# Kernel optimization log

Hardware: AMD Instinct MI355X
Metric: run time of the kernel (lower is better)

Reference implementation:

```python
import jax, jax.numpy as jnp
import numpy as np

B, N, C = 4, 2048, 81
IMG_W, IMG_H = 1024.0, 800.0
SCORE_THRESH = 0.05
NMS_THRESH = 0.5
DETS_PER_IMG = 100
BBOX_XFORM_CLIP = float(np.log(1000.0 / 16.0))
WX, WY, WW, WH = 10.0, 10.0, 5.0, 5.0


def _make_boxes(key, n):
    k1, k2, k3, k4 = jax.random.split(key, 4)
    x1 = jax.random.uniform(k1, (n,)) * (IMG_W - 60.0)
    y1 = jax.random.uniform(k2, (n,)) * (IMG_H - 60.0)
    w = 10.0 + jax.random.uniform(k3, (n,)) * 300.0
    h = 10.0 + jax.random.uniform(k4, (n,)) * 300.0
    return jnp.stack([x1, y1, jnp.minimum(x1 + w, IMG_W - 1.0), jnp.minimum(y1 + h, IMG_H - 1.0)], axis=-1)


def setup_inputs() -> dict:
    key = jax.random.key(0)
    k1, k2, k3, k4 = jax.random.split(key, 4)
    return {
        "class_logits": jax.random.normal(k1, (B * N, C), jnp.float32),
        "box_regression": jax.random.normal(k2, (B * N, C * 8), jnp.float32) * 0.5,
        "left_proposals": _make_boxes(k3, B * N),
        "right_proposals": _make_boxes(k4, B * N),
    }


def decode(rel, boxes):
    widths = boxes[:, 2] - boxes[:, 0] + 1.0
    heights = boxes[:, 3] - boxes[:, 1] + 1.0
    ctr_x = boxes[:, 0] + 0.5 * widths
    ctr_y = boxes[:, 1] + 0.5 * heights
    dx = rel[:, 0::4] / WX
    dy = rel[:, 1::4] / WY
    dw = jnp.minimum(rel[:, 2::4] / WW, BBOX_XFORM_CLIP)
    dh = jnp.minimum(rel[:, 3::4] / WH, BBOX_XFORM_CLIP)
    pcx = dx * widths[:, None] + ctr_x[:, None]
    pcy = dy * heights[:, None] + ctr_y[:, None]
    pw = jnp.exp(dw) * widths[:, None]
    ph = jnp.exp(dh) * heights[:, None]
    x1 = pcx - 0.5 * pw
    y1 = pcy - 0.5 * ph
    x2 = pcx + 0.5 * pw - 1.0
    y2 = pcy + 0.5 * ph - 1.0
    return jnp.stack([x1, y1, x2, y2], axis=-1)  # [M, C, 4]


def clip_boxes(b):
    x1 = jnp.clip(b[..., 0], 0.0, IMG_W - 1.0)
    y1 = jnp.clip(b[..., 1], 0.0, IMG_H - 1.0)
    x2 = jnp.clip(b[..., 2], 0.0, IMG_W - 1.0)
    y2 = jnp.clip(b[..., 3], 0.0, IMG_H - 1.0)
    return jnp.stack([x1, y1, x2, y2], axis=-1)


def pairwise_iou(b):
    area = jnp.clip(b[:, 2] - b[:, 0] + 1.0, 0.0) * jnp.clip(b[:, 3] - b[:, 1] + 1.0, 0.0)
    lt = jnp.maximum(b[:, None, :2], b[None, :, :2])
    rb = jnp.minimum(b[:, None, 2:], b[None, :, 2:])
    wh = jnp.clip(rb - lt + 1.0, 0.0)
    inter = wh[..., 0] * wh[..., 1]
    return inter / jnp.maximum(area[:, None] + area[None, :] - inter, 1e-6)


def nms_keep(boxes, scores):
    # greedy NMS -> boolean keep mask (fixed shape)
    n = scores.shape[0]
    order = jnp.argsort(-scores)
    iou = pairwise_iou(boxes[order])
    idx = jnp.arange(n)
    def body(i, keep):
        sup = (iou[i] > NMS_THRESH) & keep[i] & (idx > i)
        return keep & (~sup)
    keep = jax.lax.fori_loop(0, n, body, jnp.ones((n,), bool))
    return jnp.zeros((n,), bool).at[order].set(keep)


def _per_image(prob, lb, rb):
    # prob [N,C], lb/rb [N,C,4]
    labels = jnp.argmax(prob, axis=-1)
    ar = jnp.arange(prob.shape[0])
    score = prob[ar, labels]
    lbox = lb[ar, labels]
    rbox = rb[ar, labels]
    valid = (labels >= 1) & (score > SCORE_THRESH)
    s = jnp.where(valid, score, -jnp.inf)
    keep = nms_keep(lbox, s) & nms_keep(rbox, s) & valid
    ms = jnp.where(keep, score, -jnp.inf)
    kth = jax.lax.top_k(ms, DETS_PER_IMG)[0][-1]
    keep = keep & (ms >= kth)
    return lbox, rbox, score, keep


def reference(class_logits, box_regression, left_proposals, right_proposals):
    prob = jax.nn.softmax(class_logits, axis=-1)  # [B*N, C]
    reg = box_regression.reshape(-1, C, 8)
    lb = clip_boxes(decode(reg[:, :, :4].reshape(-1, C * 4), left_proposals))
    rb = clip_boxes(decode(reg[:, :, 4:].reshape(-1, C * 4), right_proposals))
    prob = prob.reshape(B, N, C)
    lb = lb.reshape(B, N, C, 4)
    rb = rb.reshape(B, N, C, 4)
    lbox, rbox, score, keep = jax.vmap(_per_image)(prob, lb, rb)
    m = keep[..., None].astype(score.dtype)
    out = jnp.concatenate([lbox * m, rbox * m, jnp.where(keep, score, 0.0)[..., None]], axis=-1)
    return out  # [B, N, 9]
```

## Files before the change

kernel.cpp:

```cpp
#include <hip/hip_runtime.h>
#include <math.h>

#define NPROP 2048
#define NIMG 4
#define NCLS 81
#define REGW 648
#define SCORE_THRESH 0.05f
#define NMS_T 0.5f
#define DETS 100
#define XC 1023.0f
#define YC 799.0f
#define BBOX_CLIP 4.135166556742356f
#define NBIN 8192
#define SEL 320
#define MAXC 512
#define WRD 8
#define TRIP 2560

typedef unsigned long long u64;

__device__ __forceinline__ float areaf(float4 v) {
  return fmaxf(v.z - v.x + 1.0f, 0.0f) * fmaxf(v.w - v.y + 1.0f, 0.0f);
}
__device__ __forceinline__ bool iou_gt(float4 a, float aa, float4 b, float ba) {
  float ix1 = fmaxf(a.x, b.x), iy1 = fmaxf(a.y, b.y);
  float ix2 = fminf(a.z, b.z), iy2 = fminf(a.w, b.w);
  float iw = fmaxf(ix2 - ix1 + 1.0f, 0.0f);
  float ih = fmaxf(iy2 - iy1 + 1.0f, 0.0f);
  float inter = iw * ih;
  return inter > NMS_T * fmaxf(aa + ba - inter, 1e-6f);
}
__device__ __forceinline__ float score_from_v(unsigned v) {
  unsigned uu = ~v;
  unsigned bits = (uu & 0x80000000u) ? (uu & 0x7fffffffu) : ~uu;
  return __uint_as_float(bits);
}
__device__ __forceinline__ float4 decode_math(float4 rr, float4 P) {
  float w  = P.z - P.x + 1.0f;
  float h  = P.w - P.y + 1.0f;
  float cx = P.x + 0.5f * w;
  float cy = P.y + 0.5f * h;
  float dx = rr.x / 10.0f;
  float dy = rr.y / 10.0f;
  float dw = fminf(rr.z / 5.0f, BBOX_CLIP);
  float dh = fminf(rr.w / 5.0f, BBOX_CLIP);
  float pcx = dx * w + cx;
  float pcy = dy * h + cy;
  float pw = expf(dw) * w;
  float ph = expf(dh) * h;
  float4 o;
  o.x = fminf(fmaxf(pcx - 0.5f * pw, 0.0f), XC);
  o.y = fminf(fmaxf(pcy - 0.5f * ph, 0.0f), YC);
  o.z = fminf(fmaxf(pcx + 0.5f * pw - 1.0f, 0.0f), XC);
  o.w = fminf(fmaxf(pcy + 0.5f * ph - 1.0f, 0.0f), YC);
  return o;
}
__device__ __forceinline__ float4 decode_side(const float* __restrict__ reg,
                                              const float4* __restrict__ props,
                                              int grow, int ci, int isR) {
  const float4 rr = *(const float4*)(reg + (size_t)grow * REGW + ci * 8 + isR * 4);
  return decode_math(rr, props[grow]);
}

__global__ __launch_bounds__(256) void score_kernel(
    const float* __restrict__ logits,
    unsigned* __restrict__ v32G, unsigned short* __restrict__ ci16G,
    int* __restrict__ doneG, float* __restrict__ out) {
  int row  = blockIdx.x * 4 + (threadIdx.x >> 6);
  int lane = threadIdx.x & 63;
  if (blockIdx.x == 0 && threadIdx.x < NIMG) doneG[threadIdx.x] = 0;
  if (blockIdx.x < 72) {
    int g = blockIdx.x * 256 + threadIdx.x;
    ((float4*)out)[g] = make_float4(0.f, 0.f, 0.f, 0.f);
  }
  const float* lr = logits + (size_t)row * NCLS;
  float a = lr[lane];
  float b = (lane < NCLS - 64) ? lr[lane + 64] : -INFINITY;
  float v; int ci;
  if (b > a) { v = b; ci = lane + 64; } else { v = a; ci = lane; }
  for (int o = 32; o; o >>= 1) {
    float ov = __shfl_xor(v, o);
    int   oc = __shfl_xor(ci, o);
    if (ov > v || (ov == v && oc < ci)) { v = ov; ci = oc; }
  }
  float e = expf(a - v) + ((lane < NCLS - 64) ? expf(b - v) : 0.0f);
  for (int o = 32; o; o >>= 1) e += __shfl_xor(e, o);
  if (lane == 0) {
    float score = 1.0f / e;
    unsigned vv = 0xFFFFFFFFu;
    if (ci >= 1 && score > SCORE_THRESH) {
      unsigned uu = __float_as_uint(score);
      uu = (uu & 0x80000000u) ? ~uu : (uu | 0x80000000u);
      vv = ~uu;
    }
    v32G[row]  = vv;
    ci16G[row] = (unsigned short)ci;
  }
}

struct P2S {
  int hist[NBIN];
  u64 keys[MAXC];
  unsigned short ssort[MAXC];
  unsigned svs[MAXC];
  float4 bx[MAXC];
  u64 mat[TRIP];
  int rnk[MAXC];
  int wsum[16];
  int Ts, cnts, ovf;
};

struct SN {
  u64 keys[NPROP];
  unsigned short sidx[NPROP];
  unsigned v32s[NPROP];
  float4 bxL[MAXC], bxR[MAXC];
  float  arL[MAXC], arR[MAXC];
  u64 keepbL[NPROP / 64], keepbR[NPROP / 64];
  u64 rowmL[64], rowmR[64];
  float4 cbL[64], cbR[64];
  float  cbLa[64], cbRa[64];
  u64 aL, aR;
  int cnt, prevCount, done, ccL, ccR, needFB;
  unsigned kthV;
};

__device__ __forceinline__ float4 get_sboxN(SN* S, const float* reg,
                                            const float4* lp4, const float4* rp4,
                                            const unsigned short* ci16G,
                                            int b, int pos, int isR) {
  if (pos < MAXC) return isR ? S->bxR[pos] : S->bxL[pos];
  int row = S->sidx[pos];
  int grow = b * NPROP + row;
  return decode_side(reg, isR ? rp4 : lp4, grow, ci16G[grow], isR);
}

__global__ __launch_bounds__(1024) void nms_fused_kernel(
    const unsigned* __restrict__ v32G, const unsigned short* __restrict__ ci16G,
    const float* __restrict__ reg, const float* __restrict__ lp,
    const float* __restrict__ rp,
    float4* __restrict__ bxRG, u64* __restrict__ keepRG,
    int* __restrict__ doneG, float* __restrict__ out) {
  constexpr unsigned SMEM = (sizeof(P2S) > sizeof(SN)) ? sizeof(P2S) : sizeof(SN);
  __shared__ __align__(16) char smemRaw[SMEM];
  P2S& P = *reinterpret_cast<P2S*>(smemRaw);
  SN&  S = *reinterpret_cast<SN*>(smemRaw);

  int b = blockIdx.x >> 1, side = blockIdx.x & 1;
  int tid = threadIdx.x, ln = tid & 63, w = tid >> 6;
  const unsigned* v32 = v32G + b * NPROP;
  const unsigned short* ci16 = ci16G + b * NPROP;

  unsigned vA0 = v32[tid], vA1 = v32[tid + 1024];
  unsigned cA0 = ci16[tid], cA1 = ci16[tid + 1024];
  if (tid == 0) { P.Ts = NBIN - 1; P.cnts = 0; P.ovf = 0; }
  for (int i = tid; i < NBIN / 4; i += 1024)
    ((int4*)P.hist)[i] = make_int4(0, 0, 0, 0);
  __syncthreads();
  if (vA0 != 0xFFFFFFFFu) atomicAdd(&P.hist[vA0 >> 19], 1);
  if (vA1 != 0xFFFFFFFFu) atomicAdd(&P.hist[vA1 >> 19], 1);
  __syncthreads();
  {
    int base = tid * 8;
    int c[8]; int acc = 0;
#pragma unroll
    for (int k = 0; k < 8; ++k) { acc += P.hist[base + k]; c[k] = acc; }
    int tot = acc, v = tot;
#pragma unroll
    for (int o = 1; o < 64; o <<= 1) { int n = __shfl_up(v, o); if (ln >= o) v += n; }
    if (ln == 63) P.wsum[w] = v;
    __syncthreads();
    if (tid < 16) {
      int x = P.wsum[tid];
#pragma unroll
      for (int o = 1; o < 16; o <<= 1) { int n = __shfl_up(x, o); if (tid >= o) x += n; }
      P.wsum[tid] = x;
    }
    __syncthreads();
    int incl = ((w > 0) ? P.wsum[w - 1] : 0) + v;
    int off = incl - tot;
    int prev = off;
#pragma unroll
    for (int k = 0; k < 8; ++k) {
      int cur = off + c[k];
      if (cur >= SEL && prev < SEL) P.Ts = base + k;
      prev = cur;
    }
  }
  __syncthreads();
  int T = P.Ts, nvTot = P.wsum[15];
  {
    unsigned vv[2] = {vA0, vA1};
    unsigned cc[2] = {cA0, cA1};
#pragma unroll
    for (int it = 0; it < 2; ++it) {
      int p = tid + it * 1024;
      unsigned v = vv[it];
      bool cand = (v != 0xFFFFFFFFu) && ((int)(v >> 19) <= T);
      u64 mb = __ballot(cand);
      int lpos = (int)__popcll(mb & ((1ull << ln) - 1ull));
      int wb = 0;
      if (ln == 0 && mb) wb = atomicAdd(&P.cnts, (int)__popcll(mb));
      wb = __shfl(wb, 0);
      if (cand) {
        int dst = wb + lpos;
        if (dst < MAXC)
          P.keys[dst] = ((u64)v << 32) | ((u64)p << 21) | ((u64)cc[it] << 14);
        else P.ovf = 1;
      }
    }
  }
  __syncthreads();
  int C1 = P.cnts;
  bool skipSel = (C1 > MAXC) || P.ovf;
  u64 A[WRD];

  if (!skipSel) {
    float4 rrD, ppD;
    unsigned myv = 0; int myp = 0;
    bool hasKey = (tid < C1);
    if (hasKey) {
      u64 k = P.keys[tid];
      myv = (unsigned)(k >> 32);
      myp = (int)((k >> 21) & 0x7FF);
      int myci = (int)((k >> 14) & 0x7F);
      int grow = b * NPROP + myp;
      ppD = ((const float4*)(side ? rp : lp))[grow];
      rrD = *(const float4*)(reg + (size_t)grow * REGW + myci * 8 + side * 4);
    }
    if (tid < 256) {
      int i0 = tid, i1 = tid + 256;
      u64 k0 = (i0 < C1) ? P.keys[i0] : ~0ull;
      u64 k1 = (i1 < C1) ? P.keys[i1] : ~0ull;
      int r0 = 0, r1 = 0;
#pragma unroll 4
      for (int j = 0; j < C1; ++j) {
        u64 kj = P.keys[j];
        r0 += (kj < k0) ? 1 : 0;
        r1 += (kj < k1) ? 1 : 0;
      }
      if (i0 < C1) P.rnk[i0] = r0;
      if (i1 < C1) P.rnk[i1] = r1;
    }
    __syncthreads();
    if (hasKey) {
      int R = P.rnk[tid];
      float4 B = decode_math(rrD, ppD);
      P.bx[R] = B;
      P.ssort[R] = (unsigned short)myp;
      P.svs[R] = myv;
      if (side) bxRG[b * MAXC + R] = B;
    }
    if (tid >= C1 && tid < MAXC) P.bx[tid] = make_float4(0.f, 0.f, 0.f, 0.f);
    __syncthreads();

    int WRDu = (C1 + 63) >> 6;
    {
      int rb = w & 7, part = w >> 3;
      int K = WRDu - rb;
      if (K > 0 && rb * 64 < C1) {
        float4 cbx[8]; float car[8];
#pragma unroll
        for (int k = 0; k < 8; ++k) {
          if (k < K) {
            cbx[k] = P.bx[(rb + k) * 64 + ln];
            car[k] = areaf(cbx[k]);
          }
        }
        u64 rw[8];
#pragma unroll
        for (int k = 0; k < 8; ++k) rw[k] = 0ull;
        int tb = 0;
        for (int kk = 0; kk < rb; ++kk) tb += ((8 - kk) | 1);
        int Sw = (8 - rb) | 1;
        int r0 = part * 32;
        int rlim = C1 - rb * 64; if (rlim > 64) rlim = 64;
        for (int j = 0; j < 32; ++j) {
          int rl = r0 + j;
          if (rl >= rlim) break;
          float4 rbx = P.bx[rb * 64 + rl];
          float rar = areaf(rbx);
#pragma unroll
          for (int k = 0; k < 8; ++k) {
            if (k < K) {
              u64 bal = __ballot(iou_gt(rbx, rar, cbx[k], car[k]));
              if (k == 0) bal &= ~((2ull << rl) - 1ull);
              rw[k] = (ln == rl) ? bal : rw[k];
            }
          }
        }
        if (ln >= r0 && ln < r0 + 32 && ln < rlim) {
          u64* myrow = &P.mat[tb * 64 + ln * Sw];
#pragma unroll
          for (int k = 0; k < 8; ++k)
            if (k < K) myrow[k] = rw[k];
        }
      }
    }
    __syncthreads();

    if (w == 0) {
#pragma unroll
      for (int t = 0; t < WRD; ++t) {
        int b0 = t * 64;
        A[t] = (C1 >= b0 + 64) ? ~0ull : (C1 > b0 ? ((1ull << (C1 - b0)) - 1ull) : 0ull);
      }
      int tbase = 0;
#pragma unroll
      for (int wb = 0; wb < WRD; ++wb) {
        if (wb * 64 < C1) {
          const int Sw = (8 - wb) | 1;
          const u64* rowp = &P.mat[tbase];
          u64 aw = A[wb];
#pragma unroll
          for (int g = 0; g < 4; ++g) {
            u64 d[16];
#pragma unroll
            for (int k = 0; k < 16; ++k) d[k] = rowp[(g * 16 + k) * Sw];
#pragma unroll
            for (int k = 0; k < 16; ++k) {
              u64 msk = 0ull - ((aw >> (g * 16 + k)) & 1ull);
              aw &= ~(msk & d[k]);
            }
          }
          A[wb] = aw;
          bool alive = (aw >> ln) & 1ull;
#pragma unroll
          for (int t = wb + 1; t < WRD; ++t) {
            if (t * 64 < C1) {
              u64 x = alive ? rowp[ln * Sw + (t - wb)] : 0ull;
#pragma unroll
              for (int o = 1; o < 64; o <<= 1)
                x |= __shfl_xor((unsigned long long)x, o);
              A[t] &= ~x;
            }
          }
        }
        tbase += 64 * ((8 - wb) | 1);
      }
      if (ln == 0 && side == 1) {
        u64* kG = keepRG + b * WRD;
#pragma unroll
        for (int t = 0; t < WRD; ++t)
          if (t * 64 < C1) kG[t] = A[t];
      }
    }
  }
  __syncthreads();

  if (side == 1) {
    if (tid == 0) {
      __threadfence();
      __hip_atomic_store(&doneG[b], 1, __ATOMIC_RELEASE, __HIP_MEMORY_SCOPE_AGENT);
    }
    return;
  }
  if (tid == 0) {
    while (__hip_atomic_load(&doneG[b], __ATOMIC_ACQUIRE,
                             __HIP_MEMORY_SCOPE_AGENT) == 0)
      __builtin_amdgcn_s_sleep(2);
    __threadfence();
  }
  __syncthreads();

  float* ob = out + (size_t)b * NPROP * 9;
  int C1e = skipSel ? 0 : C1;
  if (w == 0) {
    int before = 0;
    unsigned kth = 0;
    for (int wb = 0; wb * 64 < C1e; ++wb) {
      u64 m = A[wb] & keepRG[b * WRD + wb];
      int pos = wb * 64 + ln;
      bool bit = (m >> ln) & 1ull;
      int rank = before + (int)__popcll(m & ((1ull << ln) - 1ull));
      unsigned vv = P.svs[pos];
      u64 selm = __ballot(bit && rank == DETS - 1);
      if (selm) kth = __shfl(vv, __ffsll(selm) - 1);
      bool qual = bit && (rank < DETS || vv == kth);
      if (qual) {
        int row = P.ssort[pos];
        float4 L = P.bx[pos];
        float4 R4 = bxRG[b * MAXC + pos];
        float* orow = ob + row * 9;
        orow[0]=L.x; orow[1]=L.y; orow[2]=L.z; orow[3]=L.w;
        orow[4]=R4.x; orow[5]=R4.y; orow[6]=R4.z; orow[7]=R4.w;
        orow[8]=score_from_v(vv);
      }
      before += (int)__popcll(m);
    }
    if (ln == 0) {
      S.needFB = (before < DETS && nvTot > C1e) ? 1 : 0;
      S.cnt = 0; S.prevCount = 0; S.done = 0; S.kthV = 0u;
    }
  }
  __syncthreads();
  if (!S.needFB) return;

  const float4* lp4 = (const float4*)lp;
  const float4* rp4 = (const float4*)rp;
  float4* ob4 = (float4*)ob;
  float4 z4 = make_float4(0.f, 0.f, 0.f, 0.f);
  for (int i = tid; i < NPROP * 9 / 4; i += 1024) ob4[i] = z4;
  for (int p = tid; p < NPROP; p += 1024) {
    unsigned v = v32G[b * NPROP + p];
    S.v32s[p] = v;
    bool cand = (v != 0xFFFFFFFFu);
    u64 mb = __ballot(cand);
    int lpos = (int)__popcll(mb & ((1ull << ln) - 1ull));
    int wb = 0;
    if (ln == 0 && mb) wb = atomicAdd(&S.cnt, (int)__popcll(mb));
    wb = __shfl(wb, 0);
    if (cand) S.keys[wb + lpos] = ((u64)v << 16) | (unsigned)p;
  }
  __syncthreads();
  int C2 = S.cnt;
  int CbEnd = (C2 + 63) & ~63;
  {
    int i0 = tid, i1 = tid + 1024;
    u64 k0 = (i0 < C2) ? S.keys[i0] : ~0ull;
    u64 k1 = (i1 < C2) ? S.keys[i1] : ~0ull;
    int r0 = 0, r1 = 0;
#pragma unroll 4
    for (int j = 0; j < C2; ++j) {
      u64 kj = S.keys[j];
      r0 += (kj < k0) ? 1 : 0;
      r1 += (kj < k1) ? 1 : 0;
    }
    if (i0 < C2) S.sidx[r0] = (unsigned short)(k0 & 0xFFFFull);
    if (i1 < C2) S.sidx[r1] = (unsigned short)(k1 & 0xFFFFull);
  }
  for (int i = C2 + tid; i < CbEnd; i += 1024) S.sidx[i] = 0;
  for (int wd = tid; wd < NPROP / 64; wd += 1024) {
    int b0 = wd << 6;
    u64 mf = 0ull;
    if (C2 >= b0 + 64) mf = ~0ull;
    else if (C2 > b0)  mf = (1ull << (C2 - b0)) - 1ull;
    S.keepbL[wd] = mf; S.keepbR[wd] = mf;
  }
  __syncthreads();
  {
    int lim = min(CbEnd, MAXC);
    for (int i = tid; i < lim; i += 1024) {
      if (i < C2) {
        int row = S.sidx[i];
        int grow = b * NPROP + row;
        int ci = ci16G[grow];
        float4 L = decode_side(reg, lp4, grow, ci, 0);
        float4 R = decode_side(reg, rp4, grow, ci, 1);
        S.bxL[i] = L; S.arL[i] = areaf(L);
        S.bxR[i] = R; S.arR[i] = areaf(R);
      } else {
        S.bxL[i] = z4; S.arL[i] = 1.0f;
        S.bxR[i] = z4; S.arR[i] = 1.0f;
      }
    }
  }
  __syncthreads();
  for (int base = 0; base < CbEnd; base += 64) {
    {
      int isR = (w >= 8);
      float4 cbx = get_sboxN(&S, reg, lp4, rp4, ci16G, b, base + ln, isR);
      float car = (base + ln < MAXC) ? (isR ? S.arR[base + ln] : S.arL[base + ln])
                                     : areaf(cbx);
      int w8 = w & 7;
#pragma unroll
      for (int k = 0; k < 8; ++k) {
        int row = w8 * 8 + k;
        float4 rbx;
        rbx.x = __shfl(cbx.x, row); rbx.y = __shfl(cbx.y, row);
        rbx.z = __shfl(cbx.z, row); rbx.w = __shfl(cbx.w, row);
        float rar = __shfl(car, row);
        bool bit = (ln > row) && iou_gt(rbx, rar, cbx, car);
        u64 bal = __ballot(bit);
        if (ln == 0) { if (isR) S.rowmR[row] = bal; else S.rowmL[row] = bal; }
      }
    }
    __syncthreads();
    if (tid < 128) {
      int isR = (tid >= 64);
      u64* km = isR ? S.keepbR : S.keepbL;
      u64* rm = isR ? S.rowmR  : S.rowmL;
      u64 a = km[base >> 6];
#pragma unroll
      for (int j = 0; j < 64; ++j)
        a &= ~((0ull - ((a >> j) & 1ull)) & rm[j]);
      if (ln == 0) {
        km[base >> 6] = a;
        if (isR) { S.aR = a; S.ccR = __popcll(a); }
        else     { S.aL = a; S.ccL = __popcll(a); }
      }
      if ((a >> ln) & 1ull) {
        int pos = __popcll(a & ((1ull << ln) - 1ull));
        float4 v = get_sboxN(&S, reg, lp4, rp4, ci16G, b, base + ln, isR);
        if (isR) { S.cbR[pos] = v; S.cbRa[pos] = areaf(v); }
        else     { S.cbL[pos] = v; S.cbLa[pos] = areaf(v); }
      }
    }
    __syncthreads();
    if (w == 0) {
      u64 m = S.aL & S.aR;
      int before = S.prevCount;
      bool bit = (m >> ln) & 1ull;
      int rank = before + (int)__popcll(m & ((1ull << ln) - 1ull));
      int row = S.sidx[base + ln];
      unsigned vv = S.v32s[row];
      u64 selm = __ballot(bit && rank == DETS - 1);
      unsigned keffV = S.kthV;
      if (selm) keffV = __shfl(vv, __ffsll(selm) - 1);
      bool qual = bit && (rank < DETS || vv == keffV);
      if (qual) {
        float4 L = get_sboxN(&S, reg, lp4, rp4, ci16G, b, base + ln, 0);
        float4 R = get_sboxN(&S, reg, lp4, rp4, ci16G, b, base + ln, 1);
        float s = score_from_v(vv);
        float* orow = ob + row * 9;
        orow[0]=L.x; orow[1]=L.y; orow[2]=L.z; orow[3]=L.w;
        orow[4]=R.x; orow[5]=R.y; orow[6]=R.z; orow[7]=R.w;
        orow[8]=s;
      }
      if (ln == 0) {
        if (selm) S.kthV = keffV;
        int nc = before + (int)__popcll(m);
        S.prevCount = nc;
        if (nc >= DETS) {
          int nxt = base + 64;
          bool cont = false;
          if (nxt < C2) cont = (S.v32s[S.sidx[nxt]] == keffV);
          if (!cont) S.done = 1;
        }
      }
    } else {
      int cL = S.ccL, cR = S.ccR;
      if ((cL | cR) != 0) {
        for (int p = base + 64 + (tid - 64); p < CbEnd; p += 960) {
          float4 mbL = get_sboxN(&S, reg, lp4, rp4, ci16G, b, p, 0);
          float al = (p < MAXC) ? S.arL[p] : areaf(mbL);
          bool supL = false;
          for (int q = 0; q < cL; ++q)
            supL = supL || iou_gt(mbL, al, S.cbL[q], S.cbLa[q]);
          if (supL) atomicAnd(&S.keepbL[p >> 6], ~(1ull << (p & 63)));
          float4 mbR = get_sboxN(&S, reg, lp4, rp4, ci16G, b, p, 1);
          float ar_ = (p < MAXC) ? S.arR[p] : areaf(mbR);
          bool supR = false;
          for (int q = 0; q < cR; ++q)
            supR = supR || iou_gt(mbR, ar_, S.cbR[q], S.cbRa[q]);
          if (supR) atomicAnd(&S.keepbR[p >> 6], ~(1ull << (p & 63)));
        }
      }
    }
    __syncthreads();
    if (S.done) break;
  }
}

extern "C" void kernel_launch(void* const* d_in, const int* in_sizes, int n_in,
                              void* d_out, int out_size, void* d_ws, size_t ws_size,
                              hipStream_t stream) {
  const float* logits = (const float*)d_in[0];
  const float* reg    = (const float*)d_in[1];
  const float* lprop  = (const float*)d_in[2];
  const float* rprop  = (const float*)d_in[3];
  float* out = (float*)d_out;

  char* ws = (char*)d_ws;
  unsigned*       v32G   = (unsigned*)(ws + 0);
  unsigned short* ci16G  = (unsigned short*)(ws + 32768);
  float4*         bxRG   = (float4*)(ws + 49152);
  u64*            keepRG = (u64*)(ws + 81920);
  int*            doneG  = (int*)(ws + 82176);

  score_kernel<<<NIMG * NPROP / 4, 256, 0, stream>>>(logits, v32G, ci16G,
                                                     doneG, out);
  nms_fused_kernel<<<2 * NIMG, 1024, 0, stream>>>(v32G, ci16G, reg, lprop, rprop,
                                                  bxRG, keepRG, doneG, out);
}
```

Measured before the change: 118.2 us.

## Split fused NMS kernel into select, matrix, and finale kernels

Replaces the single 8-block fused NMS kernel, which used a global spin-wait flag between the left and right side blocks, with three kernels. A per-image select/sort kernel decodes both sides. A 64-block matrix kernel builds the IoU suppression bitmasks in parallel across row blocks. A per-image finale kernel runs both greedy scans and the output/fallback. The aim is to spread the IoU matrix work over more CUs and drop the inter-block spin synchronisation, at the cost of two extra launches and round trips through global memory for boxes and masks.

After: 118.9 us. About the same (+0.6%).

```diff
diff --git a/kernel.cpp b/kernel.cpp
--- a/kernel.cpp
+++ b/kernel.cpp
@@ -65,10 +65,9 @@
 __global__ __launch_bounds__(256) void score_kernel(
     const float* __restrict__ logits,
     unsigned* __restrict__ v32G, unsigned short* __restrict__ ci16G,
-    int* __restrict__ doneG, float* __restrict__ out) {
+    float* __restrict__ out) {
   int row  = blockIdx.x * 4 + (threadIdx.x >> 6);
   int lane = threadIdx.x & 63;
-  if (blockIdx.x == 0 && threadIdx.x < NIMG) doneG[threadIdx.x] = 0;
   if (blockIdx.x < 72) {
     int g = blockIdx.x * 256 + threadIdx.x;
     ((float4*)out)[g] = make_float4(0.f, 0.f, 0.f, 0.f);
@@ -98,17 +97,175 @@
   }
 }
 
-struct P2S {
+struct PSel {
   int hist[NBIN];
   u64 keys[MAXC];
-  unsigned short ssort[MAXC];
-  unsigned svs[MAXC];
-  float4 bx[MAXC];
-  u64 mat[TRIP];
   int rnk[MAXC];
   int wsum[16];
   int Ts, cnts, ovf;
 };
+
+__global__ __launch_bounds__(1024) void selsort_kernel(
+    const unsigned* __restrict__ v32G, const unsigned short* __restrict__ ci16G,
+    const float* __restrict__ reg, const float* __restrict__ lp,
+    const float* __restrict__ rp,
+    unsigned short* __restrict__ srowG, unsigned* __restrict__ svG,
+    float4* __restrict__ bxLG, float4* __restrict__ bxRG,
+    int* __restrict__ C1G, int* __restrict__ C2G) {
+  __shared__ PSel P;
+  int b = blockIdx.x;
+  int tid = threadIdx.x, ln = tid & 63, w = tid >> 6;
+  const unsigned* v32 = v32G + b * NPROP;
+  const unsigned short* ci16 = ci16G + b * NPROP;
+
+  unsigned vA0 = v32[tid], vA1 = v32[tid + 1024];
+  unsigned cA0 = ci16[tid], cA1 = ci16[tid + 1024];
+  if (tid == 0) { P.Ts = NBIN - 1; P.cnts = 0; P.ovf = 0; }
+  for (int i = tid; i < NBIN / 4; i += 1024)
+    ((int4*)P.hist)[i] = make_int4(0, 0, 0, 0);
+  __syncthreads();
+  if (vA0 != 0xFFFFFFFFu) atomicAdd(&P.hist[vA0 >> 19], 1);
+  if (vA1 != 0xFFFFFFFFu) atomicAdd(&P.hist[vA1 >> 19], 1);
+  __syncthreads();
+  {
+    int base = tid * 8;
+    int c[8]; int acc = 0;
+#pragma unroll
+    for (int k = 0; k < 8; ++k) { acc += P.hist[base + k]; c[k] = acc; }
+    int tot = acc, v = tot;
+#pragma unroll
+    for (int o = 1; o < 64; o <<= 1) { int n = __shfl_up(v, o); if (ln >= o) v += n; }
+    if (ln == 63) P.wsum[w] = v;
+    __syncthreads();
+    if (tid < 16) {
+      int x = P.wsum[tid];
+#pragma unroll
+      for (int o = 1; o < 16; o <<= 1) { int n = __shfl_up(x, o); if (tid >= o) x += n; }
+      P.wsum[tid] = x;
+    }
+    __syncthreads();
+    int incl = ((w > 0) ? P.wsum[w - 1] : 0) + v;
+    int off = incl - tot;
+    int prev = off;
+#pragma unroll
+    for (int k = 0; k < 8; ++k) {
+      int cur = off + c[k];
+      if (cur >= SEL && prev < SEL) P.Ts = base + k;
+      prev = cur;
+    }
+  }
+  __syncthreads();
+  int T = P.Ts, nvTot = P.wsum[15];
+  {
+    unsigned vv[2] = {vA0, vA1};
+    unsigned cc[2] = {cA0, cA1};
+#pragma unroll
+    for (int it = 0; it < 2; ++it) {
+      int p = tid + it * 1024;
+      unsigned v = vv[it];
+      bool cand = (v != 0xFFFFFFFFu) && ((int)(v >> 19) <= T);
+      u64 mb = __ballot(cand);
+      int lpos = (int)__popcll(mb & ((1ull << ln) - 1ull));
+      int wb = 0;
+      if (ln == 0 && mb) wb = atomicAdd(&P.cnts, (int)__popcll(mb));
+      wb = __shfl(wb, 0);
+      if (cand) {
+        int dst = wb + lpos;
+        if (dst < MAXC)
+          P.keys[dst] = ((u64)v << 32) | ((u64)p << 21) | ((u64)cc[it] << 14);
+        else P.ovf = 1;
+      }
+    }
+  }
+  __syncthreads();
+  int C1 = P.cnts;
+  if (C1 > MAXC || P.ovf) {
+    if (tid == 0) { C1G[b] = 0; C2G[b] = nvTot; }
+    return;
+  }
+  if (tid == 0) { C1G[b] = C1; C2G[b] = nvTot; }
+  if (tid < 256) {
+    int i0 = tid, i1 = tid + 256;
+    u64 k0 = (i0 < C1) ? P.keys[i0] : ~0ull;
+    u64 k1 = (i1 < C1) ? P.keys[i1] : ~0ull;
+    int r0 = 0, r1 = 0;
+#pragma unroll 4
+    for (int j = 0; j < C1; ++j) {
+      u64 kj = P.keys[j];
+      r0 += (kj < k0) ? 1 : 0;
+      r1 += (kj < k1) ? 1 : 0;
+    }
+    if (i0 < C1) P.rnk[i0] = r0;
+    if (i1 < C1) P.rnk[i1] = r1;
+  }
+  __syncthreads();
+  {
+    int s = tid & 511, sd = tid >> 9;
+    if (s < C1) {
+      u64 k = P.keys[s];
+      unsigned myv = (unsigned)(k >> 32);
+      int myp = (int)((k >> 21) & 0x7FF);
+      int myci = (int)((k >> 14) & 0x7F);
+      int R = P.rnk[s];
+      int grow = b * NPROP + myp;
+      float4 B = decode_side(reg, (const float4*)(sd ? rp : lp), grow, myci, sd);
+      (sd ? bxRG : bxLG)[b * MAXC + R] = B;
+      if (sd == 0) {
+        srowG[b * MAXC + R] = (unsigned short)myp;
+        svG[b * MAXC + R] = myv;
+      }
+    }
+  }
+}
+
+__global__ __launch_bounds__(256) void matrix_kernel(
+    const float4* __restrict__ bxLG, const float4* __restrict__ bxRG,
+    const int* __restrict__ C1G, u64* __restrict__ matG) {
+  __shared__ float4 bx[MAXC];
+  int id = blockIdx.x;
+  int b = id >> 4, side = (id >> 3) & 1, rb = id & 7;
+  int tid = threadIdx.x, ln = tid & 63, wv = tid >> 6;
+  int C1 = C1G[b];
+  int WRDu = (C1 + 63) >> 6;
+  if (rb >= WRDu) return;
+  const float4* src = (side ? bxRG : bxLG) + b * MAXC;
+  for (int i = tid; i < MAXC; i += 256) bx[i] = src[i];
+  __syncthreads();
+  int K = WRDu - rb;
+  float4 cbx[8]; float car[8];
+#pragma unroll
+  for (int k = 0; k < 8; ++k) {
+    if (k < K) { cbx[k] = bx[(rb + k) * 64 + ln]; car[k] = areaf(cbx[k]); }
+  }
+  u64 rw[8];
+#pragma unroll
+  for (int k = 0; k < 8; ++k) rw[k] = 0ull;
+  int tb = 0;
+  for (int kk = 0; kk < rb; ++kk) tb += ((8 - kk) | 1);
+  int Sw = (8 - rb) | 1;
+  int r0 = wv * 16;
+  int rlim = C1 - rb * 64; if (rlim > 64) rlim = 64;
+  for (int j = 0; j < 16; ++j) {
+    int rl = r0 + j;
+    if (rl >= rlim) break;
+    float4 rbx = bx[rb * 64 + rl];
+    float rar = areaf(rbx);
+#pragma unroll
+    for (int k = 0; k < 8; ++k) {
+      if (k < K) {
+        u64 bal = __ballot(iou_gt(rbx, rar, cbx[k], car[k]));
+        if (k == 0) bal &= ~((2ull << rl) - 1ull);
+        rw[k] = (ln == rl) ? bal : rw[k];
+      }
+    }
+  }
+  if (ln >= r0 && ln < r0 + 16 && ln < rlim) {
+    u64* myrow = matG + (size_t)(b * 2 + side) * TRIP + tb * 64 + ln * Sw;
+#pragma unroll
+    for (int k = 0; k < 8; ++k)
+      if (k < K) myrow[k] = rw[k];
+  }
+}
 
 struct SN {
   u64 keys[NPROP];
@@ -135,171 +292,30 @@
   return decode_side(reg, isR ? rp4 : lp4, grow, ci16G[grow], isR);
 }
 
-__global__ __launch_bounds__(1024) void nms_fused_kernel(
-    const unsigned* __restrict__ v32G, const unsigned short* __restrict__ ci16G,
+__global__ __launch_bounds__(1024) void finale_kernel(
     const float* __restrict__ reg, const float* __restrict__ lp,
-    const float* __restrict__ rp,
-    float4* __restrict__ bxRG, u64* __restrict__ keepRG,
-    int* __restrict__ doneG, float* __restrict__ out) {
-  constexpr unsigned SMEM = (sizeof(P2S) > sizeof(SN)) ? sizeof(P2S) : sizeof(SN);
-  __shared__ __align__(16) char smemRaw[SMEM];
-  P2S& P = *reinterpret_cast<P2S*>(smemRaw);
-  SN&  S = *reinterpret_cast<SN*>(smemRaw);
-
-  int b = blockIdx.x >> 1, side = blockIdx.x & 1;
-  int tid = threadIdx.x, ln = tid & 63, w = tid >> 6;
-  const unsigned* v32 = v32G + b * NPROP;
-  const unsigned short* ci16 = ci16G + b * NPROP;
-
-  unsigned vA0 = v32[tid], vA1 = v32[tid + 1024];
-  unsigned cA0 = ci16[tid], cA1 = ci16[tid + 1024];
-  if (tid == 0) { P.Ts = NBIN - 1; P.cnts = 0; P.ovf = 0; }
-  for (int i = tid; i < NBIN / 4; i += 1024)
-    ((int4*)P.hist)[i] = make_int4(0, 0, 0, 0);
-  __syncthreads();
-  if (vA0 != 0xFFFFFFFFu) atomicAdd(&P.hist[vA0 >> 19], 1);
-  if (vA1 != 0xFFFFFFFFu) atomicAdd(&P.hist[vA1 >> 19], 1);
-  __syncthreads();
-  {
-    int base = tid * 8;
-    int c[8]; int acc = 0;
-#pragma unroll
-    for (int k = 0; k < 8; ++k) { acc += P.hist[base + k]; c[k] = acc; }
-    int tot = acc, v = tot;
-#pragma unroll
-    for (int o = 1; o < 64; o <<= 1) { int n = __shfl_up(v, o); if (ln >= o) v += n; }
-    if (ln == 63) P.wsum[w] = v;
-    __syncthreads();
-    if (tid < 16) {
-      int x = P.wsum[tid];
-#pragma unroll
-      for (int o = 1; o < 16; o <<= 1) { int n = __shfl_up(x, o); if (tid >= o) x += n; }
-      P.wsum[tid] = x;
-    }
-    __syncthreads();
-    int incl = ((w > 0) ? P.wsum[w - 1] : 0) + v;
-    int off = incl - tot;
-    int prev = off;
-#pragma unroll
-    for (int k = 0; k < 8; ++k) {
-      int cur = off + c[k];
-      if (cur >= SEL && prev < SEL) P.Ts = base + k;
-      prev = cur;
-    }
-  }
-  __syncthreads();
-  int T = P.Ts, nvTot = P.wsum[15];
-  {
-    unsigned vv[2] = {vA0, vA1};
-    unsigned cc[2] = {cA0, cA1};
-#pragma unroll
-    for (int it = 0; it < 2; ++it) {
-      int p = tid + it * 1024;
-      unsigned v = vv[it];
-      bool cand = (v != 0xFFFFFFFFu) && ((int)(v >> 19) <= T);
-      u64 mb = __ballot(cand);
-      int lpos = (int)__popcll(mb & ((1ull << ln) - 1ull));
-      int wb = 0;
-      if (ln == 0 && mb) wb = atomicAdd(&P.cnts, (int)__popcll(mb));
-      wb = __shfl(wb, 0);
-      if (cand) {
-        int dst = wb + lpos;
-        if (dst < MAXC)
-          P.keys[dst] = ((u64)v << 32) | ((u64)p << 21) | ((u64)cc[it] << 14);
-        else P.ovf = 1;
-      }
-    }
-  }
-  __syncthreads();
-  int C1 = P.cnts;
-  bool skipSel = (C1 > MAXC) || P.ovf;
-  u64 A[WRD];
-
-  if (!skipSel) {
-    float4 rrD, ppD;
-    unsigned myv = 0; int myp = 0;
-    bool hasKey = (tid < C1);
-    if (hasKey) {
-      u64 k = P.keys[tid];
-      myv = (unsigned)(k >> 32);
-      myp = (int)((k >> 21) & 0x7FF);
-      int myci = (int)((k >> 14) & 0x7F);
-      int grow = b * NPROP + myp;
-      ppD = ((const float4*)(side ? rp : lp))[grow];
-      rrD = *(const float4*)(reg + (size_t)grow * REGW + myci * 8 + side * 4);
-    }
-    if (tid < 256) {
-      int i0 = tid, i1 = tid + 256;
-      u64 k0 = (i0 < C1) ? P.keys[i0] : ~0ull;
-      u64 k1 = (i1 < C1) ? P.keys[i1] : ~0ull;
-      int r0 = 0, r1 = 0;
-#pragma unroll 4
-      for (int j = 0; j < C1; ++j) {
-        u64 kj = P.keys[j];
-        r0 += (kj < k0) ? 1 : 0;
-        r1 += (kj < k1) ? 1 : 0;
-      }
-      if (i0 < C1) P.rnk[i0] = r0;
-      if (i1 < C1) P.rnk[i1] = r1;
-    }
-    __syncthreads();
-    if (hasKey) {
-      int R = P.rnk[tid];
-      float4 B = decode_math(rrD, ppD);
-      P.bx[R] = B;
-      P.ssort[R] = (unsigned short)myp;
-      P.svs[R] = myv;
-      if (side) bxRG[b * MAXC + R] = B;
-    }
-    if (tid >= C1 && tid < MAXC) P.bx[tid] = make_float4(0.f, 0.f, 0.f, 0.f);
-    __syncthreads();
-
-    int WRDu = (C1 + 63) >> 6;
-    {
-      int rb = w & 7, part = w >> 3;
-      int K = WRDu - rb;
-      if (K > 0 && rb * 64 < C1) {
-        float4 cbx[8]; float car[8];
-#pragma unroll
-        for (int k = 0; k < 8; ++k) {
-          if (k < K) {
-            cbx[k] = P.bx[(rb + k) * 64 + ln];
-            car[k] = areaf(cbx[k]);
-          }
-        }
-        u64 rw[8];
-#pragma unroll
-        for (int k = 0; k < 8; ++k) rw[k] = 0ull;
-        int tb = 0;
-        for (int kk = 0; kk < rb; ++kk) tb += ((8 - kk) | 1);
-        int Sw = (8 - rb) | 1;
-        int r0 = part * 32;
-        int rlim = C1 - rb * 64; if (rlim > 64) rlim = 64;
-        for (int j = 0; j < 32; ++j) {
-          int rl = r0 + j;
-          if (rl >= rlim) break;
-          float4 rbx = P.bx[rb * 64 + rl];
-          float rar = areaf(rbx);
-#pragma unroll
-          for (int k = 0; k < 8; ++k) {
-            if (k < K) {
-              u64 bal = __ballot(iou_gt(rbx, rar, cbx[k], car[k]));
-              if (k == 0) bal &= ~((2ull << rl) - 1ull);
-              rw[k] = (ln == rl) ? bal : rw[k];
-            }
-          }
-        }
-        if (ln >= r0 && ln < r0 + 32 && ln < rlim) {
-          u64* myrow = &P.mat[tb * 64 + ln * Sw];
-#pragma unroll
-          for (int k = 0; k < 8; ++k)
-            if (k < K) myrow[k] = rw[k];
-        }
-      }
-    }
-    __syncthreads();
-
-    if (w == 0) {
+    const float* __restrict__ rp, const unsigned* __restrict__ v32G,
+    const unsigned short* __restrict__ ci16G,
+    const unsigned short* __restrict__ srowG, const unsigned* __restrict__ svG,
+    const float4* __restrict__ bxLG, const float4* __restrict__ bxRG,
+    const int* __restrict__ C1G, const int* __restrict__ C2G,
+    const u64* __restrict__ matG, float* __restrict__ out) {
+  __shared__ u64 matL[TRIP], matR[TRIP];
+  __shared__ u64 ALs[WRD], ARs[WRD];
+  __shared__ SN S;
+  int b = blockIdx.x, tid = threadIdx.x, ln = tid & 63, w = tid >> 6;
+  float* ob = out + (size_t)b * NPROP * 9;
+  int C1 = C1G[b];
+  int nvTot = C2G[b];
+
+  if (C1 > 0) {
+    const u64* mL = matG + (size_t)(b * 2 + 0) * TRIP;
+    const u64* mR = matG + (size_t)(b * 2 + 1) * TRIP;
+    for (int i = tid; i < TRIP; i += 1024) { matL[i] = mL[i]; matR[i] = mR[i]; }
+    __syncthreads();
+    if (w < 2) {
+      const u64* matS = w ? matR : matL;
+      u64 A[WRD];
 #pragma unroll
       for (int t = 0; t < WRD; ++t) {
         int b0 = t * 64;
@@ -310,7 +326,7 @@
       for (int wb = 0; wb < WRD; ++wb) {
         if (wb * 64 < C1) {
           const int Sw = (8 - wb) | 1;
-          const u64* rowp = &P.mat[tbase];
+          const u64* rowp = &matS[tbase];
           u64 aw = A[wb];
 #pragma unroll
           for (int g = 0; g < 4; ++g) {
@@ -338,49 +354,30 @@
         }
         tbase += 64 * ((8 - wb) | 1);
       }
-      if (ln == 0 && side == 1) {
-        u64* kG = keepRG + b * WRD;
-#pragma unroll
-        for (int t = 0; t < WRD; ++t)
-          if (t * 64 < C1) kG[t] = A[t];
-      }
-    }
-  }
-  __syncthreads();
-
-  if (side == 1) {
-    if (tid == 0) {
-      __threadfence();
-      __hip_atomic_store(&doneG[b], 1, __ATOMIC_RELEASE, __HIP_MEMORY_SCOPE_AGENT);
-    }
-    return;
-  }
-  if (tid == 0) {
-    while (__hip_atomic_load(&doneG[b], __ATOMIC_ACQUIRE,
-                             __HIP_MEMORY_SCOPE_AGENT) == 0)
-      __builtin_amdgcn_s_sleep(2);
-    __threadfence();
-  }
-  __syncthreads();
-
-  float* ob = out + (size_t)b * NPROP * 9;
-  int C1e = skipSel ? 0 : C1;
+      if (ln == 0) {
+        u64* dst = w ? ARs : ALs;
+#pragma unroll
+        for (int t = 0; t < WRD; ++t) dst[t] = A[t];
+      }
+    }
+    __syncthreads();
+  }
+
   if (w == 0) {
     int before = 0;
     unsigned kth = 0;
-    for (int wb = 0; wb * 64 < C1e; ++wb) {
-      u64 m = A[wb] & keepRG[b * WRD + wb];
+    for (int wb = 0; wb * 64 < C1; ++wb) {
+      u64 m = ALs[wb] & ARs[wb];
       int pos = wb * 64 + ln;
       bool bit = (m >> ln) & 1ull;
       int rank = before + (int)__popcll(m & ((1ull << ln) - 1ull));
-      unsigned vv = P.svs[pos];
+      unsigned vv = svG[b * MAXC + pos];
       u64 selm = __ballot(bit && rank == DETS - 1);
       if (selm) kth = __shfl(vv, __ffsll(selm) - 1);
       bool qual = bit && (rank < DETS || vv == kth);
       if (qual) {
-        int row = P.ssort[pos];
-        float4 L = P.bx[pos];
-        float4 R4 = bxRG[b * MAXC + pos];
+        int row = srowG[b * MAXC + pos];
+        float4 L = bxLG[b * MAXC + pos], R4 = bxRG[b * MAXC + pos];
         float* orow = ob + row * 9;
         orow[0]=L.x; orow[1]=L.y; orow[2]=L.z; orow[3]=L.w;
         orow[4]=R4.x; orow[5]=R4.y; orow[6]=R4.z; orow[7]=R4.w;
@@ -389,7 +386,7 @@
       before += (int)__popcll(m);
     }
     if (ln == 0) {
-      S.needFB = (before < DETS && nvTot > C1e) ? 1 : 0;
+      S.needFB = (before < DETS && nvTot > C1) ? 1 : 0;
       S.cnt = 0; S.prevCount = 0; S.done = 0; S.kthV = 0u;
     }
   }
@@ -564,12 +561,21 @@
   char* ws = (char*)d_ws;
   unsigned*       v32G   = (unsigned*)(ws + 0);
   unsigned short* ci16G  = (unsigned short*)(ws + 32768);
-  float4*         bxRG   = (float4*)(ws + 49152);
-  u64*            keepRG = (u64*)(ws + 81920);
-  int*            doneG  = (int*)(ws + 82176);
-
-  score_kernel<<<NIMG * NPROP / 4, 256, 0, stream>>>(logits, v32G, ci16G,
-                                                     doneG, out);
-  nms_fused_kernel<<<2 * NIMG, 1024, 0, stream>>>(v32G, ci16G, reg, lprop, rprop,
-                                                  bxRG, keepRG, doneG, out);
-}
+  unsigned short* srowG  = (unsigned short*)(ws + 49152);
+  unsigned*       svG    = (unsigned*)(ws + 53248);
+  float4*         bxLG   = (float4*)(ws + 61440);
+  float4*         bxRG   = (float4*)(ws + 94208);
+  int*            C1G    = (int*)(ws + 126976);
+  int*            C2G    = (int*)(ws + 127040);
+  u64*            matG   = (u64*)(ws + 131072);
+
+  score_kernel  <<<NIMG * NPROP / 4, 256,  0, stream>>>(logits, v32G, ci16G, out);
+  selsort_kernel<<<NIMG,             1024, 0, stream>>>(v32G, ci16G, reg, lprop,
+                                                        rprop, srowG, svG,
+                                                        bxLG, bxRG, C1G, C2G);
+  matrix_kernel <<<NIMG * 16,        256,  0, stream>>>(bxLG, bxRG, C1G, matG);
+  finale_kernel <<<NIMG,             1024, 0, stream>>>(reg, lprop, rprop, v32G,
+                                                        ci16G, srowG, svG,
+                                                        bxLG, bxRG, C1G, C2G,
+                                                        matG, out);
+}
```
